# Performance work log

Hardware: AMD Instinct MI355X
Metric: run time of the kernel (lower is better)

The kernel has to match this reference:

```python
import jax, jax.numpy as jnp
import numpy as np

N, E, F, H, L, STEPS, VH = 50000, 800000, 64, 64, 4, 4, 64
S1 = H * L + H          # 320
VIN = S1 + H            # 384
REG_IN = S1 + VH + 1    # 385
EPS = 1e-5


def setup_inputs() -> dict:
    key = jax.random.key(0)
    ks = iter(jax.random.split(key, 64))
    nk = lambda: next(ks)

    def w(shape):
        fan_in = shape[-2] if len(shape) > 1 else shape[-1]
        return jax.random.normal(nk(), shape, jnp.float32) / np.float32(np.sqrt(fan_in))

    def b(shape):
        return 0.01 * jax.random.normal(nk(), shape, jnp.float32)

    return {
        "x": jax.random.normal(nk(), (N, F), jnp.float32),
        "edge_index": jax.random.randint(nk(), (2, E), 0, N, jnp.int32),
        "W_in": w((F, H)), "b_in": b((H,)),
        # stacked per-layer SAGEConv params (all layers are H->H)
        "sage_Wl": w((L, H, H)), "sage_bl": b((L, H)), "sage_Wr": w((L, H, H)),
        "bn_gamma": jnp.ones((L, H), jnp.float32) + 0.1 * jax.random.normal(nk(), (L, H), jnp.float32),
        "bn_beta": b((L, H)),
        "bn_mean": 0.1 * jax.random.normal(nk(), (L, H), jnp.float32),
        "bn_var": 1.0 + 0.5 * jax.random.uniform(nk(), (L, H), jnp.float32),
        "vW_l": w((VIN, VH)), "vb_l": b((VH,)), "vW_r": w((VIN, VH)),
        "vbn_gamma": jnp.ones((VH,), jnp.float32) + 0.1 * jax.random.normal(nk(), (VH,), jnp.float32),
        "vbn_beta": b((VH,)),
        "vbn_mean": 0.1 * jax.random.normal(nk(), (VH,), jnp.float32),
        "vbn_var": 1.0 + 0.5 * jax.random.uniform(nk(), (VH,), jnp.float32),
        "W_mu": w((VH, VH)), "b_mu": b((VH,)),
        "W_lv": w((VH, VH)), "b_lv": b((VH,)),
        "rank_W1": w((VH, H)), "rank_b1": b((H,)),
        "rank_W2": w((H, 1)), "rank_b2": b((1,)),
        "reg_W1": w((REG_IN, H)), "reg_b1": b((H,)),
        "reg_W2": w((H, H // 2)), "reg_b2": b((H // 2,)),
        "reg_W3": w((H // 2, 1)), "reg_b3": b((1,)),
    }


def reference(x, edge_index, W_in, b_in, sage_Wl, sage_bl, sage_Wr,
              bn_gamma, bn_beta, bn_mean, bn_var,
              vW_l, vb_l, vW_r, vbn_gamma, vbn_beta, vbn_mean, vbn_var,
              W_mu, b_mu, W_lv, b_lv,
              rank_W1, rank_b1, rank_W2, rank_b2,
              reg_W1, reg_b1, reg_W2, reg_b2, reg_W3, reg_b3):
    n = x.shape[0]
    row, col = edge_index[0], edge_index[1]
    ones_e = jnp.ones(row.shape, x.dtype)

    def sage(h, Wl, bl, Wr):
        # mean aggregation of source features at destination nodes (PyG SAGEConv)
        agg = jax.ops.segment_sum(h[row], col, num_segments=n)          # [N, Fin]
        cnt = jax.ops.segment_sum(ones_e, col, num_segments=n)          # in-degree
        mean = agg / jnp.maximum(cnt, 1.0)[:, None]
        return mean @ Wl + bl + h @ Wr

    def bn(h, g, be, m, v):
        return (h - m) * jax.lax.rsqrt(v + EPS) * g + be

    inp_skip = x @ W_in + b_in
    h = x
    layer_outputs = []
    for i in range(L):  # fixed small layer loop; res_proj is Identity (in_feats == hidden)
        h_fwd = jax.nn.relu(bn(sage(h, sage_Wl[i], sage_bl[i], sage_Wr[i]),
                               bn_gamma[i], bn_beta[i], bn_mean[i], bn_var[i]))
        h = h_fwd + h
        layer_outputs.append(h)
    stage1 = jnp.concatenate(layer_outputs + [inp_skip], axis=1)        # [N, 320]

    # path_agg: row-degree-normalized scatter, iterated path_steps times
    deg = jnp.maximum(jax.ops.segment_sum(ones_e, row, num_segments=n), 1.0)
    norm = (1.0 / deg)[row]                                             # [E]
    out = h
    for _ in range(STEPS):
        out = jax.ops.segment_sum(out[row] * norm[:, None], col, num_segments=n)

    vgae_in = jnp.concatenate([stage1, out], axis=1)                    # [N, 384]
    v = jax.nn.relu(bn(sage(vgae_in, vW_l, vb_l, vW_r),
                       vbn_gamma, vbn_beta, vbn_mean, vbn_var))
    mu = v @ W_mu + b_mu
    logvar = v @ W_lv + b_lv
    z = mu  # eval mode: no reparameterization noise

    rank_score = (jax.nn.relu(z @ rank_W1 + rank_b1) @ rank_W2 + rank_b2)[:, 0]

    reg_in = jnp.concatenate([stage1, z, rank_score[:, None]], axis=1)  # [N, 385]
    h1 = jax.nn.relu(reg_in @ reg_W1 + reg_b1)
    h2 = jax.nn.relu(h1 @ reg_W2 + reg_b2)
    preds = h2 @ reg_W3 + reg_b3
    return preds, rank_score, mu, logvar
```

## Files before the change

### kernel.cpp

```cpp
#include <hip/hip_runtime.h>
#include <cstdint>
#include <cstddef>

#define NN 50000
#define EE 800000
#define CAP 64
#define EPS_BN 1e-5f

typedef short  s16x8 __attribute__((ext_vector_type(8)));
typedef ushort u16x8 __attribute__((ext_vector_type(8)));
typedef float  f32x4 __attribute__((ext_vector_type(4)));

#define MFMA16(a, b, c) __builtin_amdgcn_mfma_f32_16x16x32_bf16((a), (b), (c), 0, 0, 0)

__device__ inline ushort f2bf(float f){
  uint32_t u = __float_as_uint(f);
  uint32_t r = (u + 0x7FFFu + ((u >> 16) & 1u)) >> 16;
  return (ushort)r;
}
__device__ inline float bf2f(ushort u){ return __uint_as_float((uint32_t)u << 16); }


__global__ void k_outdeg(const int* __restrict__ row, int* __restrict__ outdeg){
  int e = blockIdx.x * blockDim.x + threadIdx.x;
  if (e < EE) atomicAdd(&outdeg[row[e]], 1);
}

__global__ void k_invdeg(const int* __restrict__ outdeg, float* __restrict__ invdeg){
  int n = blockIdx.x * blockDim.x + threadIdx.x;
  if (n < NN) invdeg[n] = 1.0f / fmaxf((float)outdeg[n], 1.0f);
}

__global__ void k_fill(const int* __restrict__ row, const int* __restrict__ col,
                       int* __restrict__ incnt, ushort* __restrict__ bsrc16){
  int e = blockIdx.x * blockDim.x + threadIdx.x;
  if (e >= EE) return;
  int r = row[e], c = col[e];
  int j = atomicAdd(&incnt[c], 1);
  if (j < CAP) bsrc16[(size_t)c * CAP + j] = (ushort)r;
}


__global__ void k_cvt(const float* __restrict__ src, ushort* __restrict__ dst, int n4){
  int i = blockIdx.x * blockDim.x + threadIdx.x;
  int stride = gridDim.x * blockDim.x;
  for (; i < n4; i += stride){
    float4 v = ((const float4*)src)[i];
    ushort4 u = {f2bf(v.x), f2bf(v.y), f2bf(v.z), f2bf(v.w)};
    ((ushort4*)dst)[i] = u;
  }
}


struct FJob { const float* srcA; const float* srcB; ushort* dst;
              int NF; int NCT; int P; int mode; int splitVal; };
struct FJobs { FJob j[10]; };

__global__ void k_conv(FJobs J){
  FJob jb = J.j[blockIdx.x];
  int total = jb.NCT * jb.P * 1024;
  for (int idx = threadIdx.x + blockIdx.y * 256; idx < total; idx += 256 * gridDim.y){
    int j = idx & 7, lane = (idx >> 3) & 63, ks = (idx >> 9) & 1;
    int rest = idx >> 10;
    int p = rest % jb.P, ct = rest / jb.P;
    int col = ct * 16 + (lane & 15);
    int k   = p * 64 + ks * 32 + (lane >> 4) * 8 + j;
    const float* s = jb.srcA;
    int sc = col, sk = k;
    if (jb.mode == 1 && k   >= jb.splitVal){ s = jb.srcB; sk = k   - jb.splitVal; }
    if (jb.mode == 2 && col >= jb.splitVal){ s = jb.srcB; sc = col - jb.splitVal; }
    jb.dst[idx] = f2bf(s[(size_t)sk * jb.NF + sc]);
  }
}


__global__ void __launch_bounds__(256) k_agg(const ushort* __restrict__ hin,
                                             ushort* __restrict__ out,
                                             const ushort* __restrict__ bsrc16,
                                             const float* __restrict__ invdeg,
                                             const int* __restrict__ incnt,
                                             int use_norm){
  __shared__ int   sidx[4][CAP + 16];
  __shared__ float swgt[4][CAP + 16];
  int wib  = threadIdx.x >> 6;
  int lane = threadIdx.x & 63;
  int wid  = blockIdx.x * 4 + wib;
  bool valid = wid < NN;
  int cnt  = valid ? incnt[wid] : 0;
  int cntb = min(cnt, CAP);
  if (valid){
    int src = (lane < cntb) ? (int)bsrc16[(size_t)wid * CAP + lane] : 0;
    float w = 0.f;
    if (lane < cntb)
      w = use_norm ? invdeg[src] : (1.0f / fmaxf((float)cnt, 1.f));
    sidx[wib][lane] = src;
    swgt[wib][lane] = w;
    if (lane < 16){ sidx[wib][CAP + lane] = 0; swgt[wib][CAP + lane] = 0.f; }
  }
  __syncthreads();
  if (!valid) return;

  int g  = lane >> 3;
  int fl = lane & 7;
  float accf[8] = {0,0,0,0,0,0,0,0};
  for (int e0 = 0; e0 < cntb; e0 += 16){
    int ea = e0 + g, eb = e0 + g + 8;
    int   sa = sidx[wib][ea], sb = sidx[wib][eb];
    float wa = swgt[wib][ea], wb = swgt[wib][eb];
    u16x8 va = *(const u16x8*)(hin + (size_t)sa * 64 + fl * 8);
    u16x8 vb = *(const u16x8*)(hin + (size_t)sb * 64 + fl * 8);
    #pragma unroll
    for (int j = 0; j < 8; ++j){
      accf[j] = fmaf(wa, bf2f(va[j]), accf[j]);
      accf[j] = fmaf(wb, bf2f(vb[j]), accf[j]);
    }
  }
  #pragma unroll
  for (int m = 8; m < 64; m <<= 1){
    #pragma unroll
    for (int j = 0; j < 8; ++j) accf[j] += __shfl_xor(accf[j], m);
  }
  if (lane < 8){
    u16x8 o;
    #pragma unroll
    for (int j = 0; j < 8; ++j) o[j] = f2bf(accf[j]);
    *(u16x8*)(out + (size_t)wid * 64 + lane * 8) = o;
  }
}


template<int P, int NCT>
__device__ inline void gemm_direct(const ushort* const* pieces,
                                   const ushort* __restrict__ WB,
                                   int rowbase, f32x4* acc){
  int lane = threadIdx.x & 63;
  int q = lane >> 4, r16 = lane & 15;
  int ar = rowbase + r16; ar = (ar < NN) ? ar : (NN - 1);
  const ushort* wl = WB + lane * 8;
  #pragma unroll
  for (int p = 0; p < P; ++p){
    const ushort* src = pieces[p] + (size_t)ar * 64 + q * 8;
    #pragma unroll
    for (int ks = 0; ks < 2; ++ks){
      s16x8 a = *(const s16x8*)(src + ks * 32);
      #pragma unroll
      for (int ct = 0; ct < NCT; ++ct){
        s16x8 b = *(const s16x8*)(wl + (((ct * P + p) * 2 + ks) << 9));
        acc[ct] = MFMA16(a, b, acc[ct]);
      }
    }
  }
}

__global__ void __launch_bounds__(256) k_skip(const ushort* __restrict__ xb,
                                              const ushort* __restrict__ WT,
                                              const float* __restrict__ bias,
                                              ushort* __restrict__ outb){
  int lane = threadIdx.x & 63, wv = threadIdx.x >> 6, q = lane >> 4, r16 = lane & 15;
  int rowbase = blockIdx.x * 64 + wv * 16;
  const ushort* pieces[1] = {xb};
  f32x4 acc[4] = {};
  gemm_direct<1, 4>(pieces, WT, rowbase, acc);
  #pragma unroll
  for (int ct = 0; ct < 4; ++ct){
    int col = ct * 16 + r16;
    float b = bias[col];
    #pragma unroll
    for (int r = 0; r < 4; ++r){
      int row = rowbase + q * 4 + r;
      if (row < NN) outb[(size_t)row * 64 + col] = f2bf(acc[ct][r] + b);
    }
  }
}

__global__ void __launch_bounds__(256) k_sage_m(const ushort* __restrict__ meanb,
                                                const ushort* __restrict__ hb,
                                                const ushort* __restrict__ WT,
                                                const float* __restrict__ bl,
                                                const float* __restrict__ g,
                                                const float* __restrict__ be,
                                                const float* __restrict__ m_,
                                                const float* __restrict__ var_,
                                                ushort* __restrict__ houtb){
  int lane = threadIdx.x & 63, wv = threadIdx.x >> 6, q = lane >> 4, r16 = lane & 15;
  int rowbase = blockIdx.x * 64 + wv * 16;
  const ushort* pieces[2] = {meanb, hb};
  f32x4 acc[4] = {};
  gemm_direct<2, 4>(pieces, WT, rowbase, acc);
  #pragma unroll
  for (int ct = 0; ct < 4; ++ct){
    int col = ct * 16 + r16;
    float sc = g[col] * rsqrtf(var_[col] + EPS_BN);
    float sh = be[col] - m_[col] * sc;
    float bb = bl[col];
    #pragma unroll
    for (int r = 0; r < 4; ++r){
      int row = rowbase + q * 4 + r;
      if (row < NN){
        float t = (acc[ct][r] + bb) * sc + sh;
        float hv = bf2f(hb[(size_t)row * 64 + col]);
        houtb[(size_t)row * 64 + col] = f2bf(fmaxf(t, 0.f) + hv);
      }
    }
  }
}

__global__ void __launch_bounds__(256) k_yr(const ushort* __restrict__ x0, const ushort* __restrict__ x1,
                                            const ushort* __restrict__ x2, const ushort* __restrict__ x3,
                                            const ushort* __restrict__ x4, const ushort* __restrict__ x5,
                                            const ushort* __restrict__ WT, const float* __restrict__ vbl,
                                            ushort* __restrict__ Y, ushort* __restrict__ R){
  int lane = threadIdx.x & 63, wv = threadIdx.x >> 6, q = lane >> 4, r16 = lane & 15;
  int rowbase = blockIdx.x * 64 + wv * 16;
  const ushort* pieces[6] = {x0, x1, x2, x3, x4, x5};
  f32x4 acc[8] = {};
  gemm_direct<6, 8>(pieces, WT, rowbase, acc);
  #pragma unroll
  for (int ct = 0; ct < 8; ++ct){
    int col = ct * 16 + r16;
    bool isR = col >= 64;
    int c2 = isR ? (col - 64) : col;
    float b = isR ? vbl[c2] : 0.f;
    ushort* dst = isR ? R : Y;
    #pragma unroll
    for (int r = 0; r < 4; ++r){
      int row = rowbase + q * 4 + r;
      if (row < NN) dst[(size_t)row * 64 + c2] = f2bf(acc[ct][r] + b);
    }
  }
}

__global__ void __launch_bounds__(256) k_mulv_m(const ushort* __restrict__ Yagg,
                                                const ushort* __restrict__ Rb,
                                                const float* __restrict__ vg,
                                                const float* __restrict__ vbe,
                                                const float* __restrict__ vm,
                                                const float* __restrict__ vvar,
                                                const ushort* __restrict__ WT,
                                                const float* __restrict__ bmu,
                                                const float* __restrict__ blv,
                                                float* __restrict__ muf, float* __restrict__ lvf,
                                                ushort* __restrict__ mub){
  __shared__ float ssc[64], ssh[64];
  int t = threadIdx.x;
  if (t < 64){
    float sc = vg[t] * rsqrtf(vvar[t] + EPS_BN);
    ssc[t] = sc; ssh[t] = vbe[t] - vm[t] * sc;
  }
  __syncthreads();
  int lane = t & 63, wv = t >> 6, q = lane >> 4, r16 = lane & 15;
  int rowbase = blockIdx.x * 64 + wv * 16;
  int ar = rowbase + r16; ar = (ar < NN) ? ar : (NN - 1);
  const ushort* wl = WT + lane * 8;
  f32x4 acc[8] = {};
  #pragma unroll
  for (int ks = 0; ks < 2; ++ks){
    int k0 = ks * 32 + q * 8;
    u16x8 y  = *(const u16x8*)(Yagg + (size_t)ar * 64 + k0);
    u16x8 rv = *(const u16x8*)(Rb   + (size_t)ar * 64 + k0);
    s16x8 a;
    #pragma unroll
    for (int j = 0; j < 8; ++j){
      float tv = (bf2f(y[j]) + bf2f(rv[j])) * ssc[k0 + j] + ssh[k0 + j];
      a[j] = (short)f2bf(fmaxf(tv, 0.f));
    }
    #pragma unroll
    for (int ct = 0; ct < 8; ++ct){
      s16x8 b = *(const s16x8*)(wl + (((ct * 1) * 2 + ks) << 9));
      acc[ct] = MFMA16(a, b, acc[ct]);
    }
  }
  #pragma unroll
  for (int ct = 0; ct < 8; ++ct){
    int col = ct * 16 + r16;
    bool isL = col >= 64;
    int c2 = isL ? (col - 64) : col;
    float bb = isL ? blv[c2] : bmu[c2];
    #pragma unroll
    for (int r = 0; r < 4; ++r){
      int row = rowbase + q * 4 + r;
      if (row < NN){
        float v = acc[ct][r] + bb;
        if (isL) lvf[(size_t)row * 64 + c2] = v;
        else { muf[(size_t)row * 64 + c2] = v; mub[(size_t)row * 64 + c2] = f2bf(v); }
      }
    }
  }
}

__global__ void __launch_bounds__(256) k_rank_m(const ushort* __restrict__ mub,
                                                const ushort* __restrict__ WT,
                                                const float* __restrict__ rb1,
                                                const float* __restrict__ rW2,
                                                const float* __restrict__ rb2,
                                                float* __restrict__ rout){
  int lane = threadIdx.x & 63, wv = threadIdx.x >> 6, q = lane >> 4, r16 = lane & 15;
  int rowbase = blockIdx.x * 64 + wv * 16;
  const ushort* pieces[1] = {mub};
  f32x4 acc[4] = {};
  gemm_direct<1, 4>(pieces, WT, rowbase, acc);
  float val[4] = {0.f, 0.f, 0.f, 0.f};
  #pragma unroll
  for (int ct = 0; ct < 4; ++ct){
    int col = ct * 16 + r16;
    float b1 = rb1[col], w2 = rW2[col];
    #pragma unroll
    for (int r = 0; r < 4; ++r)
      val[r] += fmaxf(acc[ct][r] + b1, 0.f) * w2;
  }
  #pragma unroll
  for (int r = 0; r < 4; ++r){
    #pragma unroll
    for (int m = 1; m < 16; m <<= 1) val[r] += __shfl_xor(val[r], m);
  }
  if (r16 == 0){
    float b2 = rb2[0];
    #pragma unroll
    for (int r = 0; r < 4; ++r){
      int row = rowbase + q * 4 + r;
      if (row < NN) rout[row] = val[r] + b2;
    }
  }
}

__global__ void __launch_bounds__(256) k_reg1(const ushort* __restrict__ x0, const ushort* __restrict__ x1,
                                              const ushort* __restrict__ x2, const ushort* __restrict__ x3,
                                              const ushort* __restrict__ x4, const ushort* __restrict__ x5,
                                              const float* __restrict__ rank,
                                              const ushort* __restrict__ WT,
                                              const float* __restrict__ gW1,
                                              const float* __restrict__ gb1,
                                              ushort* __restrict__ h1b){
  int lane = threadIdx.x & 63, wv = threadIdx.x >> 6, q = lane >> 4, r16 = lane & 15;
  int rowbase = blockIdx.x * 64 + wv * 16;
  const ushort* pieces[6] = {x0, x1, x2, x3, x4, x5};
  f32x4 acc[4] = {};
  gemm_direct<6, 4>(pieces, WT, rowbase, acc);
  float rk[4];
  #pragma unroll
  for (int r = 0; r < 4; ++r){
    int row = rowbase + q * 4 + r;
    rk[r] = (row < NN) ? rank[row] : 0.f;
  }
  #pragma unroll
  for (int ct = 0; ct < 4; ++ct){
    int col = ct * 16 + r16;
    float b1 = gb1[col];
    float w384 = gW1[384 * 64 + col];
    #pragma unroll
    for (int r = 0; r < 4; ++r){
      int row = rowbase + q * 4 + r;
      if (row < NN)
        h1b[(size_t)row * 64 + col] = f2bf(fmaxf(acc[ct][r] + b1 + rk[r] * w384, 0.f));
    }
  }
}

__global__ void __launch_bounds__(256) k_reg2(const ushort* __restrict__ h1b,
                                              const ushort* __restrict__ WT,
                                              const float* __restrict__ gb2,
                                              const float* __restrict__ gW3,
                                              const float* __restrict__ gb3,
                                              float* __restrict__ preds){
  int lane = threadIdx.x & 63, wv = threadIdx.x >> 6, q = lane >> 4, r16 = lane & 15;
  int rowbase = blockIdx.x * 64 + wv * 16;
  const ushort* pieces[1] = {h1b};
  f32x4 acc[2] = {};
  gemm_direct<1, 2>(pieces, WT, rowbase, acc);
  float val[4] = {0.f, 0.f, 0.f, 0.f};
  #pragma unroll
  for (int ct = 0; ct < 2; ++ct){
    int col = ct * 16 + r16;
    float b2 = gb2[col], w3 = gW3[col];
    #pragma unroll
    for (int r = 0; r < 4; ++r)
      val[r] += fmaxf(acc[ct][r] + b2, 0.f) * w3;
  }
  #pragma unroll
  for (int r = 0; r < 4; ++r){
    #pragma unroll
    for (int m = 1; m < 16; m <<= 1) val[r] += __shfl_xor(val[r], m);
  }
  if (r16 == 0){
    float b3 = gb3[0];
    #pragma unroll
    for (int r = 0; r < 4; ++r){
      int row = rowbase + q * 4 + r;
      if (row < NN) preds[row] = val[r] + b3;
    }
  }
}


extern "C" void kernel_launch(void* const* d_in, const int* in_sizes, int n_in,
                              void* d_out, int out_size, void* d_ws, size_t ws_size,
                              hipStream_t stream){
  const float* x    = (const float*)d_in[0];
  const int*   eidx = (const int*)d_in[1];
  const int* row = eidx;
  const int* col = eidx + EE;
  const float* W_in = (const float*)d_in[2];
  const float* b_in = (const float*)d_in[3];
  const float* sWl  = (const float*)d_in[4];
  const float* sbl  = (const float*)d_in[5];
  const float* sWr  = (const float*)d_in[6];
  const float* bng  = (const float*)d_in[7];
  const float* bnb  = (const float*)d_in[8];
  const float* bnm  = (const float*)d_in[9];
  const float* bnv  = (const float*)d_in[10];
  const float* vWl  = (const float*)d_in[11];
  const float* vbl  = (const float*)d_in[12];
  const float* vWr  = (const float*)d_in[13];
  const float* vg   = (const float*)d_in[14];
  const float* vbe  = (const float*)d_in[15];
  const float* vm   = (const float*)d_in[16];
  const float* vvar = (const float*)d_in[17];
  const float* Wmu  = (const float*)d_in[18];
  const float* bmu  = (const float*)d_in[19];
  const float* Wlv  = (const float*)d_in[20];
  const float* blv  = (const float*)d_in[21];
  const float* rW1  = (const float*)d_in[22];
  const float* rb1  = (const float*)d_in[23];
  const float* rW2  = (const float*)d_in[24];
  const float* rb2  = (const float*)d_in[25];
  const float* gW1  = (const float*)d_in[26];
  const float* gb1  = (const float*)d_in[27];
  const float* gW2  = (const float*)d_in[28];
  const float* gb2  = (const float*)d_in[29];
  const float* gW3  = (const float*)d_in[30];
  const float* gb3  = (const float*)d_in[31];

  float* preds = (float*)d_out;
  float* rank  = preds + NN;
  float* mu    = rank + NN;
  float* lv    = mu + (size_t)NN * 64;

  char* w = (char*)d_ws;
  auto alloc = [&](size_t bytes) -> char* {
    char* p = w; w += (bytes + 255) & ~(size_t)255; return p;
  };
  int*    outdeg = (int*)alloc((size_t)NN * 4);
  int*    incnt  = (int*)alloc((size_t)NN * 4);
  float*  invdeg = (float*)alloc((size_t)NN * 4);
  ushort* bsrc16 = (ushort*)alloc((size_t)NN * CAP * 2);
  const size_t FB = (size_t)NN * 64 * 2;
  ushort* xb    = (ushort*)alloc(FB);
  ushort* skipb = (ushort*)alloc(FB);
  ushort* hb[4];
  for (int i = 0; i < 4; ++i) hb[i] = (ushort*)alloc(FB);
  ushort* meanb = (ushort*)alloc(FB);
  ushort* pa    = (ushort*)alloc(FB);
  ushort* pb    = (ushort*)alloc(FB);
  ushort* Yb    = (ushort*)alloc(FB);
  ushort* Rb    = (ushort*)alloc(FB);
  ushort* mub   = (ushort*)alloc(FB);
  ushort* skipW = (ushort*)alloc(4 * 1024 * 2);
  ushort* sageW = (ushort*)alloc(4 * 8 * 1024 * 2);
  ushort* yrW   = (ushort*)alloc(48 * 1024 * 2);
  ushort* mulvW = (ushort*)alloc(8 * 1024 * 2);
  ushort* rankW = (ushort*)alloc(4 * 1024 * 2);
  ushort* regW1 = (ushort*)alloc(24 * 1024 * 2);
  ushort* regW2 = (ushort*)alloc(2 * 1024 * 2);

  hipMemsetAsync(outdeg, 0, (size_t)NN * 4, stream);
  hipMemsetAsync(incnt,  0, (size_t)NN * 4, stream);

  const int EB = (EE + 255) / 256;
  k_outdeg<<<EB, 256, 0, stream>>>(row, outdeg);
  k_invdeg<<<(NN + 255) / 256, 256, 0, stream>>>(outdeg, invdeg);
  k_fill  <<<EB, 256, 0, stream>>>(row, col, incnt, bsrc16);

  FJobs J;
  auto job = [&](int i, const float* sA, const float* sB, ushort* d,
                 int NF, int NCT, int P, int mode, int splitVal){
    J.j[i] = {sA, sB, d, NF, NCT, P, mode, splitVal};
  };
  job(0, W_in, nullptr, skipW, 64, 4, 1, 0, 0);
  for (int i = 0; i < 4; ++i)
    job(1 + i, sWl + i * 4096, sWr + i * 4096, sageW + i * 8192, 64, 4, 2, 1, 64);
  job(5, vWl, vWr, yrW,   64, 8, 6, 2, 64);
  job(6, Wmu, Wlv, mulvW, 64, 8, 1, 2, 64);
  job(7, rW1, nullptr, rankW, 64, 4, 1, 0, 0);
  job(8, gW1, nullptr, regW1, 64, 4, 6, 0, 0);
  job(9, gW2, nullptr, regW2, 32, 2, 1, 0, 0);
  k_conv<<<dim3(10, 8), 256, 0, stream>>>(J);

  k_cvt<<<1024, 256, 0, stream>>>(x, xb, NN * 64 / 4);

  const int GB = (NN + 63) / 64;
  k_skip<<<GB, 256, 0, stream>>>(xb, skipW, b_in, skipb);

  const int AGG_B = (NN + 3) / 4;
  const ushort* hprev = xb;
  for (int i = 0; i < 4; ++i){
    k_agg<<<AGG_B, 256, 0, stream>>>(hprev, meanb, bsrc16, invdeg, incnt, 0);
    k_sage_m<<<GB, 256, 0, stream>>>(meanb, hprev, sageW + i * 8192, sbl + i * 64,
                                     bng + i * 64, bnb + i * 64, bnm + i * 64, bnv + i * 64, hb[i]);
    hprev = hb[i];
  }

  k_agg<<<AGG_B, 256, 0, stream>>>(hb[3], pa, bsrc16, invdeg, incnt, 1);
  k_agg<<<AGG_B, 256, 0, stream>>>(pa, pb, bsrc16, invdeg, incnt, 1);
  k_agg<<<AGG_B, 256, 0, stream>>>(pb, pa, bsrc16, invdeg, incnt, 1);
  k_agg<<<AGG_B, 256, 0, stream>>>(pa, pb, bsrc16, invdeg, incnt, 1);

  k_yr<<<GB, 256, 0, stream>>>(hb[0], hb[1], hb[2], hb[3], skipb, pb, yrW, vbl, Yb, Rb);
  k_agg<<<AGG_B, 256, 0, stream>>>(Yb, meanb, bsrc16, invdeg, incnt, 0);
  k_mulv_m<<<GB, 256, 0, stream>>>(meanb, Rb, vg, vbe, vm, vvar, mulvW, bmu, blv, mu, lv, mub);
  k_rank_m<<<GB, 256, 0, stream>>>(mub, rankW, rb1, rW2, rb2, rank);
  k_reg1<<<GB, 256, 0, stream>>>(hb[0], hb[1], hb[2], hb[3], skipb, mub, rank,
                                 regW1, gW1, gb1, pa);
  k_reg2<<<GB, 256, 0, stream>>>(pa, regW2, gb2, gW3, gb3, preds);
}
```

Measured before the change: 529.0 us.

## Fuse mean aggregation into SAGE and mu/logvar GEMM kernels; merge degree prep

The neighbor mean aggregation is folded into the SAGE layer kernel and into the mu/logvar kernel. Each block gathers its 64 nodes' neighbor means into shared memory and feeds them straight into the MFMA, so the intermediate mean buffer no longer makes a global round trip and five launches disappear. The out-degree and in-bucket fill kernels are merged, and inverse degree is now computed on the fly instead of stored. In exchange, each block serialises 16 nodes per wave in the gather, which lowers parallelism and adds shared-memory pressure. It also adds an outdeg load plus a divide per edge in the path aggregation.

Result: slower. 565.8 us (+6.9%).

```diff
diff --git a/kernel.cpp b/kernel.cpp
--- a/kernel.cpp
+++ b/kernel.cpp
@@ -21,21 +21,13 @@
 __device__ inline float bf2f(ushort u){ return __uint_as_float((uint32_t)u << 16); }
 
 
-__global__ void k_outdeg(const int* __restrict__ row, int* __restrict__ outdeg){
-  int e = blockIdx.x * blockDim.x + threadIdx.x;
-  if (e < EE) atomicAdd(&outdeg[row[e]], 1);
-}
-
-__global__ void k_invdeg(const int* __restrict__ outdeg, float* __restrict__ invdeg){
-  int n = blockIdx.x * blockDim.x + threadIdx.x;
-  if (n < NN) invdeg[n] = 1.0f / fmaxf((float)outdeg[n], 1.0f);
-}
-
-__global__ void k_fill(const int* __restrict__ row, const int* __restrict__ col,
-                       int* __restrict__ incnt, ushort* __restrict__ bsrc16){
+__global__ void k_prep(const int* __restrict__ row, const int* __restrict__ col,
+                       int* __restrict__ outdeg, int* __restrict__ incnt,
+                       ushort* __restrict__ bsrc16){
   int e = blockIdx.x * blockDim.x + threadIdx.x;
   if (e >= EE) return;
   int r = row[e], c = col[e];
+  atomicAdd(&outdeg[r], 1);
   int j = atomicAdd(&incnt[c], 1);
   if (j < CAP) bsrc16[(size_t)c * CAP + j] = (ushort)r;
 }
@@ -77,7 +69,7 @@
 __global__ void __launch_bounds__(256) k_agg(const ushort* __restrict__ hin,
                                              ushort* __restrict__ out,
                                              const ushort* __restrict__ bsrc16,
-                                             const float* __restrict__ invdeg,
+                                             const int* __restrict__ outdeg,
                                              const int* __restrict__ incnt,
                                              int use_norm){
   __shared__ int   sidx[4][CAP + 16];
@@ -92,7 +84,8 @@
     int src = (lane < cntb) ? (int)bsrc16[(size_t)wid * CAP + lane] : 0;
     float w = 0.f;
     if (lane < cntb)
-      w = use_norm ? invdeg[src] : (1.0f / fmaxf((float)cnt, 1.f));
+      w = use_norm ? (1.0f / fmaxf((float)outdeg[src], 1.f))
+                   : (1.0f / fmaxf((float)cnt, 1.f));
     sidx[wib][lane] = src;
     swgt[wib][lane] = w;
     if (lane < 16){ sidx[wib][CAP + lane] = 0; swgt[wib][CAP + lane] = 0.f; }
@@ -129,6 +122,115 @@
 }
 
 
+__device__ inline void block_agg_mean(const ushort* __restrict__ hsrc,
+                                      const ushort* __restrict__ bsrc16,
+                                      const int* __restrict__ incnt,
+                                      int base, ushort* sidx ,
+                                      ushort* sMean, float* scw, int* scnt){
+  int wib = threadIdx.x >> 6, lane = threadIdx.x & 63;
+  #pragma unroll 1
+  for (int ni = 0; ni < 16; ++ni){
+    int nrow = wib * 16 + ni;
+    int node = base + nrow;
+    int cnt  = (node < NN) ? incnt[node] : 0;
+    int cntb = min(cnt, CAP);
+    if (lane == 0){ scnt[nrow] = cntb; scw[nrow] = 1.0f / fmaxf((float)cnt, 1.f); }
+    ushort* si = sidx + nrow * (CAP + 16);
+    si[lane] = (node < NN && lane < cntb) ? bsrc16[(size_t)node * CAP + lane] : (ushort)0;
+    if (lane < 16) si[CAP + lane] = 0;
+  }
+  int g8 = lane >> 3, fl = lane & 7;
+  #pragma unroll 1
+  for (int ni = 0; ni < 16; ++ni){
+    int nrow = wib * 16 + ni;
+    int cntb = scnt[nrow];
+    float w  = scw[nrow];
+    const ushort* si = sidx + nrow * (CAP + 16);
+    float accf[8] = {0,0,0,0,0,0,0,0};
+    for (int e0 = 0; e0 < cntb; e0 += 16){
+      int ea = e0 + g8, eb = ea + 8;
+      int   sa = si[ea], sb = si[eb];
+      float wa = (ea < cntb) ? w : 0.f;
+      float wb = (eb < cntb) ? w : 0.f;
+      u16x8 va = *(const u16x8*)(hsrc + (size_t)sa * 64 + fl * 8);
+      u16x8 vb = *(const u16x8*)(hsrc + (size_t)sb * 64 + fl * 8);
+      #pragma unroll
+      for (int j = 0; j < 8; ++j){
+        accf[j] = fmaf(wa, bf2f(va[j]), accf[j]);
+        accf[j] = fmaf(wb, bf2f(vb[j]), accf[j]);
+      }
+    }
+    #pragma unroll
+    for (int m = 8; m < 64; m <<= 1){
+      #pragma unroll
+      for (int j = 0; j < 8; ++j) accf[j] += __shfl_xor(accf[j], m);
+    }
+    if (lane < 8){
+      u16x8 o;
+      #pragma unroll
+      for (int j = 0; j < 8; ++j) o[j] = f2bf(accf[j]);
+      *(u16x8*)(sMean + nrow * 72 + lane * 8) = o;
+    }
+  }
+}
+
+__global__ void __launch_bounds__(256) k_sage_f(const ushort* __restrict__ hb,
+                                                const ushort* __restrict__ WT,
+                                                const ushort* __restrict__ bsrc16,
+                                                const int* __restrict__ incnt,
+                                                const float* __restrict__ bl,
+                                                const float* __restrict__ g,
+                                                const float* __restrict__ be,
+                                                const float* __restrict__ m_,
+                                                const float* __restrict__ var_,
+                                                ushort* __restrict__ houtb){
+  __shared__ ushort sidx[64 * (CAP + 16)];
+  __shared__ __align__(16) ushort sMean[64 * 72];
+  __shared__ float scw[64];
+  __shared__ int   scnt[64];
+  int base = blockIdx.x * 64;
+  block_agg_mean(hb, bsrc16, incnt, base, sidx, sMean, scw, scnt);
+  __syncthreads();
+
+  int lane = threadIdx.x & 63, wv = threadIdx.x >> 6, q = lane >> 4, r16 = lane & 15;
+  int wrow = wv * 16 + r16;
+  int ar = base + wrow; ar = (ar < NN) ? ar : (NN - 1);
+  const ushort* wl = WT + lane * 8;
+  f32x4 acc[4] = {};
+  #pragma unroll
+  for (int ks = 0; ks < 2; ++ks){
+    s16x8 a0 = *(const s16x8*)(sMean + wrow * 72 + ks * 32 + q * 8);
+    #pragma unroll
+    for (int ct = 0; ct < 4; ++ct){
+      s16x8 b = *(const s16x8*)(wl + (((ct * 2 + 0) * 2 + ks) << 9));
+      acc[ct] = MFMA16(a0, b, acc[ct]);
+    }
+    s16x8 a1 = *(const s16x8*)(hb + (size_t)ar * 64 + ks * 32 + q * 8);
+    #pragma unroll
+    for (int ct = 0; ct < 4; ++ct){
+      s16x8 b = *(const s16x8*)(wl + (((ct * 2 + 1) * 2 + ks) << 9));
+      acc[ct] = MFMA16(a1, b, acc[ct]);
+    }
+  }
+  #pragma unroll
+  for (int ct = 0; ct < 4; ++ct){
+    int col = ct * 16 + r16;
+    float sc = g[col] * rsqrtf(var_[col] + EPS_BN);
+    float sh = be[col] - m_[col] * sc;
+    float bb = bl[col];
+    #pragma unroll
+    for (int r = 0; r < 4; ++r){
+      int row = base + wv * 16 + q * 4 + r;
+      if (row < NN){
+        float t = (acc[ct][r] + bb) * sc + sh;
+        float hv = bf2f(hb[(size_t)row * 64 + col]);
+        houtb[(size_t)row * 64 + col] = f2bf(fmaxf(t, 0.f) + hv);
+      }
+    }
+  }
+}
+
+
 template<int P, int NCT>
 __device__ inline void gemm_direct(const ushort* const* pieces,
                                    const ushort* __restrict__ WB,
@@ -169,38 +271,6 @@
     for (int r = 0; r < 4; ++r){
       int row = rowbase + q * 4 + r;
       if (row < NN) outb[(size_t)row * 64 + col] = f2bf(acc[ct][r] + b);
-    }
-  }
-}
-
-__global__ void __launch_bounds__(256) k_sage_m(const ushort* __restrict__ meanb,
-                                                const ushort* __restrict__ hb,
-                                                const ushort* __restrict__ WT,
-                                                const float* __restrict__ bl,
-                                                const float* __restrict__ g,
-                                                const float* __restrict__ be,
-                                                const float* __restrict__ m_,
-                                                const float* __restrict__ var_,
-                                                ushort* __restrict__ houtb){
-  int lane = threadIdx.x & 63, wv = threadIdx.x >> 6, q = lane >> 4, r16 = lane & 15;
-  int rowbase = blockIdx.x * 64 + wv * 16;
-  const ushort* pieces[2] = {meanb, hb};
-  f32x4 acc[4] = {};
-  gemm_direct<2, 4>(pieces, WT, rowbase, acc);
-  #pragma unroll
-  for (int ct = 0; ct < 4; ++ct){
-    int col = ct * 16 + r16;
-    float sc = g[col] * rsqrtf(var_[col] + EPS_BN);
-    float sh = be[col] - m_[col] * sc;
-    float bb = bl[col];
-    #pragma unroll
-    for (int r = 0; r < 4; ++r){
-      int row = rowbase + q * 4 + r;
-      if (row < NN){
-        float t = (acc[ct][r] + bb) * sc + sh;
-        float hv = bf2f(hb[(size_t)row * 64 + col]);
-        houtb[(size_t)row * 64 + col] = f2bf(fmaxf(t, 0.f) + hv);
-      }
     }
   }
 }
@@ -230,8 +300,10 @@
   }
 }
 
-__global__ void __launch_bounds__(256) k_mulv_m(const ushort* __restrict__ Yagg,
+__global__ void __launch_bounds__(256) k_mulv_f(const ushort* __restrict__ Yb,
                                                 const ushort* __restrict__ Rb,
+                                                const ushort* __restrict__ bsrc16,
+                                                const int* __restrict__ incnt,
                                                 const float* __restrict__ vg,
                                                 const float* __restrict__ vbe,
                                                 const float* __restrict__ vm,
@@ -241,23 +313,30 @@
                                                 const float* __restrict__ blv,
                                                 float* __restrict__ muf, float* __restrict__ lvf,
                                                 ushort* __restrict__ mub){
+  __shared__ ushort sidx[64 * (CAP + 16)];
+  __shared__ __align__(16) ushort sMean[64 * 72];
+  __shared__ float scw[64];
+  __shared__ int   scnt[64];
   __shared__ float ssc[64], ssh[64];
   int t = threadIdx.x;
   if (t < 64){
     float sc = vg[t] * rsqrtf(vvar[t] + EPS_BN);
     ssc[t] = sc; ssh[t] = vbe[t] - vm[t] * sc;
   }
+  int base = blockIdx.x * 64;
+  block_agg_mean(Yb, bsrc16, incnt, base, sidx, sMean, scw, scnt);
   __syncthreads();
+
   int lane = t & 63, wv = t >> 6, q = lane >> 4, r16 = lane & 15;
-  int rowbase = blockIdx.x * 64 + wv * 16;
-  int ar = rowbase + r16; ar = (ar < NN) ? ar : (NN - 1);
+  int wrow = wv * 16 + r16;
+  int ar = base + wrow; ar = (ar < NN) ? ar : (NN - 1);
   const ushort* wl = WT + lane * 8;
   f32x4 acc[8] = {};
   #pragma unroll
   for (int ks = 0; ks < 2; ++ks){
     int k0 = ks * 32 + q * 8;
-    u16x8 y  = *(const u16x8*)(Yagg + (size_t)ar * 64 + k0);
-    u16x8 rv = *(const u16x8*)(Rb   + (size_t)ar * 64 + k0);
+    u16x8 y  = *(const u16x8*)(sMean + wrow * 72 + k0);
+    u16x8 rv = *(const u16x8*)(Rb + (size_t)ar * 64 + k0);
     s16x8 a;
     #pragma unroll
     for (int j = 0; j < 8; ++j){
@@ -266,7 +345,7 @@
     }
     #pragma unroll
     for (int ct = 0; ct < 8; ++ct){
-      s16x8 b = *(const s16x8*)(wl + (((ct * 1) * 2 + ks) << 9));
+      s16x8 b = *(const s16x8*)(wl + ((ct * 2 + ks) << 9));
       acc[ct] = MFMA16(a, b, acc[ct]);
     }
   }
@@ -278,7 +357,7 @@
     float bb = isL ? blv[c2] : bmu[c2];
     #pragma unroll
     for (int r = 0; r < 4; ++r){
-      int row = rowbase + q * 4 + r;
+      int row = base + wv * 16 + q * 4 + r;
       if (row < NN){
         float v = acc[ct][r] + bb;
         if (isL) lvf[(size_t)row * 64 + c2] = v;
@@ -441,14 +520,12 @@
   };
   int*    outdeg = (int*)alloc((size_t)NN * 4);
   int*    incnt  = (int*)alloc((size_t)NN * 4);
-  float*  invdeg = (float*)alloc((size_t)NN * 4);
   ushort* bsrc16 = (ushort*)alloc((size_t)NN * CAP * 2);
   const size_t FB = (size_t)NN * 64 * 2;
   ushort* xb    = (ushort*)alloc(FB);
   ushort* skipb = (ushort*)alloc(FB);
   ushort* hb[4];
   for (int i = 0; i < 4; ++i) hb[i] = (ushort*)alloc(FB);
-  ushort* meanb = (ushort*)alloc(FB);
   ushort* pa    = (ushort*)alloc(FB);
   ushort* pb    = (ushort*)alloc(FB);
   ushort* Yb    = (ushort*)alloc(FB);
@@ -466,9 +543,7 @@
   hipMemsetAsync(incnt,  0, (size_t)NN * 4, stream);
 
   const int EB = (EE + 255) / 256;
-  k_outdeg<<<EB, 256, 0, stream>>>(row, outdeg);
-  k_invdeg<<<(NN + 255) / 256, 256, 0, stream>>>(outdeg, invdeg);
-  k_fill  <<<EB, 256, 0, stream>>>(row, col, incnt, bsrc16);
+  k_prep<<<EB, 256, 0, stream>>>(row, col, outdeg, incnt, bsrc16);
 
   FJobs J;
   auto job = [&](int i, const float* sA, const float* sB, ushort* d,
@@ -490,23 +565,23 @@
   const int GB = (NN + 63) / 64;
   k_skip<<<GB, 256, 0, stream>>>(xb, skipW, b_in, skipb);
 
-  const int AGG_B = (NN + 3) / 4;
   const ushort* hprev = xb;
   for (int i = 0; i < 4; ++i){
-    k_agg<<<AGG_B, 256, 0, stream>>>(hprev, meanb, bsrc16, invdeg, incnt, 0);
-    k_sage_m<<<GB, 256, 0, stream>>>(meanb, hprev, sageW + i * 8192, sbl + i * 64,
-                                     bng + i * 64, bnb + i * 64, bnm + i * 64, bnv + i * 64, hb[i]);
+    k_sage_f<<<GB, 256, 0, stream>>>(hprev, sageW + i * 8192, bsrc16, incnt,
+                                     sbl + i * 64, bng + i * 64, bnb + i * 64,
+                                     bnm + i * 64, bnv + i * 64, hb[i]);
     hprev = hb[i];
   }
 
-  k_agg<<<AGG_B, 256, 0, stream>>>(hb[3], pa, bsrc16, invdeg, incnt, 1);
-  k_agg<<<AGG_B, 256, 0, stream>>>(pa, pb, bsrc16, invdeg, incnt, 1);
-  k_agg<<<AGG_B, 256, 0, stream>>>(pb, pa, bsrc16, invdeg, incnt, 1);
-  k_agg<<<AGG_B, 256, 0, stream>>>(pa, pb, bsrc16, invdeg, incnt, 1);
+  const int AGG_B = (NN + 3) / 4;
+  k_agg<<<AGG_B, 256, 0, stream>>>(hb[3], pa, bsrc16, outdeg, incnt, 1);
+  k_agg<<<AGG_B, 256, 0, stream>>>(pa, pb, bsrc16, outdeg, incnt, 1);
+  k_agg<<<AGG_B, 256, 0, stream>>>(pb, pa, bsrc16, outdeg, incnt, 1);
+  k_agg<<<AGG_B, 256, 0, stream>>>(pa, pb, bsrc16, outdeg, incnt, 1);
 
   k_yr<<<GB, 256, 0, stream>>>(hb[0], hb[1], hb[2], hb[3], skipb, pb, yrW, vbl, Yb, Rb);
-  k_agg<<<AGG_B, 256, 0, stream>>>(Yb, meanb, bsrc16, invdeg, incnt, 0);
-  k_mulv_m<<<GB, 256, 0, stream>>>(meanb, Rb, vg, vbe, vm, vvar, mulvW, bmu, blv, mu, lv, mub);
+  k_mulv_f<<<GB, 256, 0, stream>>>(Yb, Rb, bsrc16, incnt, vg, vbe, vm, vvar,
+                                   mulvW, bmu, blv, mu, lv, mub);
   k_rank_m<<<GB, 256, 0, stream>>>(mub, rankW, rb1, rW2, rb2, rank);
   k_reg1<<<GB, 256, 0, stream>>>(hb[0], hb[1], hb[2], hb[3], skipb, mub, rank,
                                  regW1, gW1, gb1, pa);
```
